# Kernel optimization log

Hardware: AMD Instinct MI355X
Metric: run time of the kernel (lower is better)

The kernel has to match this reference:

```python
import math
import jax, jax.numpy as jnp
import numpy as np

B, T, E = 1, 4096, 768
H, D = 12, 64
RA_WINDOW = 512
INIT_GATES = (2.2, 0.6, 0.1)


def setup_inputs() -> dict:
    key = jax.random.key(0)
    ks = jax.random.split(key, 6)
    x = jax.random.normal(ks[0], (B, T, E), dtype=jnp.float32)
    # Linear weights stored as [in, out] (math-equivalent to torch's x @ W.T)
    s = 1.0 / math.sqrt(E)
    Wq = jax.random.normal(ks[1], (E, H * D), dtype=jnp.float32) * s
    Wk = jax.random.normal(ks[2], (E, H * D), dtype=jnp.float32) * s
    Wv = jax.random.normal(ks[3], (E, H * D), dtype=jnp.float32) * s
    Wo = jax.random.normal(ks[4], (H * D, E), dtype=jnp.float32) * s
    gates = jnp.tile(jnp.asarray(INIT_GATES, dtype=jnp.float32)[None, :], (H, 1))  # [H,3]
    u = jax.random.normal(ks[5], (H, D), dtype=jnp.float32) * 0.02
    return {"x": x, "Wq": Wq, "Wk": Wk, "Wv": Wv, "Wo": Wo, "gates": gates, "u": u}


def reference(x, Wq, Wk, Wv, Wo, gates, u):
    # projections -> [B,H,T,D]
    def proj(W):
        return (x @ W).reshape(B, T, H, D).transpose(0, 2, 1, 3)
    Q, K, V = proj(Wq), proj(Wk), proj(Wv)

    S = jnp.einsum('bhtd,bhsd->bhts', Q, K) / math.sqrt(D)  # [B,H,T,T]

    w = jax.nn.softmax(gates, axis=-1)  # [H,3]
    w_std = w[:, 0][None, :, None, None]
    w_rec = w[:, 1][None, :, None, None]
    w_disc = w[:, 2][None, :, None, None]

    logits = w_std * S + w_rec * jnp.swapaxes(S, -2, -1)

    # discoverability column bias from K via per-head u
    d_raw = jnp.einsum('bhtd,hd->bht', K, u)
    d = d_raw - jnp.mean(d_raw, axis=-1, keepdims=True)
    logits = logits + w_disc * d[:, :, None, :]

    # causal banded mask
    idx = jnp.arange(T)
    mask = (idx[None, :] <= idx[:, None]) & (jnp.abs(idx[None, :] - idx[:, None]) <= RA_WINDOW)
    logits = jnp.where(mask[None, None, :, :], logits, -jnp.inf)

    attn = jax.nn.softmax(logits, axis=-1)
    ctx = jnp.einsum('bhts,bhsd->bhtd', attn, V)
    out = ctx.transpose(0, 2, 1, 3).reshape(B, T, H * D) @ Wo
    return (out, attn)
```

## Files before the change

kernel.cpp:

```cpp
#include <hip/hip_runtime.h>
#include <cstddef>

#define T_LEN 4096
#define EMB 768
#define NH 12
#define HD 64
#define WIN 512

#define GBM 128
#define GBN 128
#define GBK 16

__global__ __launch_bounds__(256) void gemm3_f32(const float* __restrict__ A,
                                                 const float* __restrict__ B0,
                                                 const float* __restrict__ B1,
                                                 const float* __restrict__ B2,
                                                 float* __restrict__ C0,
                                                 float* __restrict__ C1,
                                                 float* __restrict__ C2,
                                                 int M, int N, int K) {
    __shared__ float As[GBK][GBM + 4];
    __shared__ float Bs[GBK][GBN + 4];
    const int tid = threadIdx.x;
    const int bm = blockIdx.y * GBM;
    const int bn = blockIdx.x * GBN;
    const float* __restrict__ B = (blockIdx.z == 0) ? B0 : (blockIdx.z == 1) ? B1 : B2;
    float* __restrict__ C = (blockIdx.z == 0) ? C0 : (blockIdx.z == 1) ? C1 : C2;

    const int ty = (tid >> 4) << 2;
    const int tx = (tid & 15) << 2;

    const int ar = tid >> 1;
    const int ac = (tid & 1) << 3;
    const int br = tid >> 4;
    const int bc = (tid & 15) << 3;

    float acc[8][8] = {};

    for (int k0 = 0; k0 < K; k0 += GBK) {
        const float4 a0 = *(const float4*)&A[(size_t)(bm + ar) * K + k0 + ac];
        const float4 a1 = *(const float4*)&A[(size_t)(bm + ar) * K + k0 + ac + 4];
        As[ac + 0][ar] = a0.x; As[ac + 1][ar] = a0.y; As[ac + 2][ar] = a0.z; As[ac + 3][ar] = a0.w;
        As[ac + 4][ar] = a1.x; As[ac + 5][ar] = a1.y; As[ac + 6][ar] = a1.z; As[ac + 7][ar] = a1.w;
        *(float4*)&Bs[br][bc]     = *(const float4*)&B[(size_t)(k0 + br) * N + bn + bc];
        *(float4*)&Bs[br][bc + 4] = *(const float4*)&B[(size_t)(k0 + br) * N + bn + bc + 4];
        __syncthreads();
#pragma unroll
        for (int k = 0; k < GBK; ++k) {
            const float4 a0v = *(const float4*)&As[k][ty];
            const float4 a1v = *(const float4*)&As[k][ty + 64];
            const float4 b0v = *(const float4*)&Bs[k][tx];
            const float4 b1v = *(const float4*)&Bs[k][tx + 64];
            const float av[8] = {a0v.x, a0v.y, a0v.z, a0v.w, a1v.x, a1v.y, a1v.z, a1v.w};
            const float bv[8] = {b0v.x, b0v.y, b0v.z, b0v.w, b1v.x, b1v.y, b1v.z, b1v.w};
#pragma unroll
            for (int i = 0; i < 8; ++i)
#pragma unroll
                for (int j = 0; j < 8; ++j)
                    acc[i][j] += av[i] * bv[j];
        }
        __syncthreads();
    }
#pragma unroll
    for (int i = 0; i < 8; ++i) {
        const int r = bm + ty + ((i < 4) ? i : (60 + i));
        *(float4*)&C[(size_t)r * N + bn + tx]      = make_float4(acc[i][0], acc[i][1], acc[i][2], acc[i][3]);
        *(float4*)&C[(size_t)r * N + bn + tx + 64] = make_float4(acc[i][4], acc[i][5], acc[i][6], acc[i][7]);
    }
}

__global__ __launch_bounds__(256) void dbias_kernel(const float* __restrict__ K,
                                                    const float* __restrict__ u,
                                                    float* __restrict__ d_bias) {
    const int h = blockIdx.x;
    const int tid = threadIdx.x;
    __shared__ __align__(16) float us[HD];
    __shared__ float dr[T_LEN];
    __shared__ float red[256];
    if (tid < HD) us[tid] = u[h * HD + tid];
    __syncthreads();
    const float4* u4 = (const float4*)us;
    float lsum = 0.f;
    for (int t = tid; t < T_LEN; t += 256) {
        const float4* Kp = (const float4*)&K[(size_t)t * EMB + h * HD];
        float acc = 0.f;
#pragma unroll
        for (int i = 0; i < HD / 4; ++i) {
            float4 k4 = Kp[i];
            float4 uu = u4[i];
            acc += k4.x * uu.x + k4.y * uu.y + k4.z * uu.z + k4.w * uu.w;
        }
        dr[t] = acc;
        lsum += acc;
    }
    red[tid] = lsum;
    __syncthreads();
    for (int off = 128; off > 0; off >>= 1) {
        if (tid < off) red[tid] += red[tid + off];
        __syncthreads();
    }
    const float mean = red[0] * (1.0f / (float)T_LEN);
    __syncthreads();
    for (int t = tid; t < T_LEN; t += 256) {
        d_bias[h * T_LEN + t] = dr[t] - mean;
    }
}

__global__ __launch_bounds__(256) void attn_band_kernel(const float* __restrict__ Q,
                                                        const float* __restrict__ K,
                                                        const float* __restrict__ V,
                                                        const float* __restrict__ d_bias,
                                                        const float* __restrict__ gates,
                                                        float* __restrict__ attn,
                                                        float* __restrict__ ctx,
                                                        float* __restrict__ row_max,
                                                        float* __restrict__ row_invden) {
    const int t0  = blockIdx.x << 6;
    const int h   = blockIdx.y;
    const int tid = threadIdx.x;
    const int tm  = (tid >> 4) << 2;
    const int tn4 = (tid & 15) << 2;
    const int lm  = tid >> 2;
    const int lk  = (tid & 3) << 2;

    __shared__ __align__(16) float QT[64][68];
    __shared__ __align__(16) float KT[64][68];
    __shared__ __align__(16) float Cc[64][68];
    __shared__ __align__(16) float Qs[64][68];

    const float g0 = gates[h * 3 + 0];
    const float g1 = gates[h * 3 + 1];
    const float g2 = gates[h * 3 + 2];
    const float gm = fmaxf(g0, fmaxf(g1, g2));
    const float e0 = __expf(g0 - gm), e1 = __expf(g1 - gm), e2 = __expf(g2 - gm);
    const float gi = 1.0f / (e0 + e1 + e2);
    const float w_std = e0 * gi * 0.125f;
    const float w_rec = e1 * gi * 0.125f;
    const float w_disc = e2 * gi;

    {
        const float* Qp = Q + (size_t)(t0 + lm) * EMB + h * HD + lk;
        const float* Kp = K + (size_t)(t0 + lm) * EMB + h * HD + lk;
#pragma unroll
        for (int it = 0; it < 4; ++it) {
            float4 a = *(const float4*)(Qp + 16 * it);
            QT[lk + 16 * it + 0][lm] = a.x;
            QT[lk + 16 * it + 1][lm] = a.y;
            QT[lk + 16 * it + 2][lm] = a.z;
            QT[lk + 16 * it + 3][lm] = a.w;
            float4 b = *(const float4*)(Kp + 16 * it);
            KT[lk + 16 * it + 0][lm] = b.x;
            KT[lk + 16 * it + 1][lm] = b.y;
            KT[lk + 16 * it + 2][lm] = b.z;
            KT[lk + 16 * it + 3][lm] = b.w;
        }
    }

    const int s_base = (t0 - WIN > 0) ? (t0 - WIN) : 0;
    const int nch = ((t0 + 64) - s_base) >> 6;

    float rm[4], rden[4], acc[4][4];
#pragma unroll
    for (int i = 0; i < 4; ++i) {
        rm[i] = -1e30f;
        rden[i] = 0.f;
#pragma unroll
        for (int j = 0; j < 4; ++j) acc[i][j] = 0.f;
    }

    for (int c = 0; c < nch; ++c) {
        const int s0 = s_base + (c << 6);
        __syncthreads();
        {
            const float* Kp = K + (size_t)(s0 + lm) * EMB + h * HD + lk;
            const float* Qp = Q + (size_t)(s0 + lm) * EMB + h * HD + lk;
#pragma unroll
            for (int it = 0; it < 4; ++it) {
                float4 b = *(const float4*)(Kp + 16 * it);
                Cc[lk + 16 * it + 0][lm] = b.x;
                Cc[lk + 16 * it + 1][lm] = b.y;
                Cc[lk + 16 * it + 2][lm] = b.z;
                Cc[lk + 16 * it + 3][lm] = b.w;
                float4 q = *(const float4*)(Qp + 16 * it);
                Qs[lk + 16 * it + 0][lm] = q.x;
                Qs[lk + 16 * it + 1][lm] = q.y;
                Qs[lk + 16 * it + 2][lm] = q.z;
                Qs[lk + 16 * it + 3][lm] = q.w;
            }
        }
        __syncthreads();

        float m1[4][4] = {};
        float m2[4][4] = {};
#pragma unroll 8
        for (int k = 0; k < 64; ++k) {
            const float4 aq = *(const float4*)&QT[k][tm];
            const float4 bk = *(const float4*)&Cc[k][tn4];
            const float4 ak = *(const float4*)&KT[k][tm];
            const float4 bq = *(const float4*)&Qs[k][tn4];
            m1[0][0] += aq.x * bk.x; m1[0][1] += aq.x * bk.y; m1[0][2] += aq.x * bk.z; m1[0][3] += aq.x * bk.w;
            m1[1][0] += aq.y * bk.x; m1[1][1] += aq.y * bk.y; m1[1][2] += aq.y * bk.z; m1[1][3] += aq.y * bk.w;
            m1[2][0] += aq.z * bk.x; m1[2][1] += aq.z * bk.y; m1[2][2] += aq.z * bk.z; m1[2][3] += aq.z * bk.w;
            m1[3][0] += aq.w * bk.x; m1[3][1] += aq.w * bk.y; m1[3][2] += aq.w * bk.z; m1[3][3] += aq.w * bk.w;
            m2[0][0] += ak.x * bq.x; m2[0][1] += ak.x * bq.y; m2[0][2] += ak.x * bq.z; m2[0][3] += ak.x * bq.w;
            m2[1][0] += ak.y * bq.x; m2[1][1] += ak.y * bq.y; m2[1][2] += ak.y * bq.z; m2[1][3] += ak.y * bq.w;
            m2[2][0] += ak.z * bq.x; m2[2][1] += ak.z * bq.y; m2[2][2] += ak.z * bq.z; m2[2][3] += ak.z * bq.w;
            m2[3][0] += ak.w * bq.x; m2[3][1] += ak.w * bq.y; m2[3][2] += ak.w * bq.z; m2[3][3] += ak.w * bq.w;
        }

        const float4 db = *(const float4*)&d_bias[h * T_LEN + s0 + tn4];
        float l[4][4];
#pragma unroll
        for (int i = 0; i < 4; ++i) {
            const int t = t0 + tm + i;
            const float dbv[4] = {db.x, db.y, db.z, db.w};
#pragma unroll
            for (int j = 0; j < 4; ++j) {
                const int s = s0 + tn4 + j;
                float lv = w_std * m1[i][j] + w_rec * m2[i][j] + w_disc * dbv[j];
                const bool valid = (s <= t) && (s >= t - WIN);
                l[i][j] = valid ? lv : -1e30f;
            }
            *(float4*)&attn[((size_t)(h * T_LEN + t)) * T_LEN + s0 + tn4] =
                make_float4(l[i][0], l[i][1], l[i][2], l[i][3]);
        }
        float cmx[4];
#pragma unroll
        for (int i = 0; i < 4; ++i)
            cmx[i] = fmaxf(fmaxf(l[i][0], l[i][1]), fmaxf(l[i][2], l[i][3]));
#pragma unroll
        for (int off = 1; off < 16; off <<= 1) {
#pragma unroll
            for (int i = 0; i < 4; ++i) cmx[i] = fmaxf(cmx[i], __shfl_xor(cmx[i], off));
        }
        float cs[4];
#pragma unroll
        for (int i = 0; i < 4; ++i) {
            const float nm = fmaxf(rm[i], cmx[i]);
            const float f = __expf(rm[i] - nm);
            float s = 0.f;
#pragma unroll
            for (int j = 0; j < 4; ++j) {
                const float p = __expf(l[i][j] - nm);
                l[i][j] = p;
                s += p;
            }
            cs[i] = s;
            rm[i] = nm;
            rden[i] *= f;
#pragma unroll
            for (int j = 0; j < 4; ++j) acc[i][j] *= f;
        }
#pragma unroll
        for (int off = 1; off < 16; off <<= 1) {
#pragma unroll
            for (int i = 0; i < 4; ++i) cs[i] += __shfl_xor(cs[i], off);
        }
#pragma unroll
        for (int i = 0; i < 4; ++i) rden[i] += cs[i];

        __syncthreads();
#pragma unroll
        for (int i = 0; i < 4; ++i)
#pragma unroll
            for (int j = 0; j < 4; ++j)
                Cc[tn4 + j][tm + i] = l[i][j];
        {
            const float* Vp = V + (size_t)(s0 + lm) * EMB + h * HD + lk;
#pragma unroll
            for (int it = 0; it < 4; ++it)
                *(float4*)&Qs[lm][lk + 16 * it] = *(const float4*)(Vp + 16 * it);
        }
        __syncthreads();

#pragma unroll 16
        for (int k = 0; k < 64; ++k) {
            const float4 av = *(const float4*)&Cc[k][tm];
            const float4 bv = *(const float4*)&Qs[k][tn4];
            acc[0][0] += av.x * bv.x; acc[0][1] += av.x * bv.y; acc[0][2] += av.x * bv.z; acc[0][3] += av.x * bv.w;
            acc[1][0] += av.y * bv.x; acc[1][1] += av.y * bv.y; acc[1][2] += av.y * bv.z; acc[1][3] += av.y * bv.w;
            acc[2][0] += av.z * bv.x; acc[2][1] += av.z * bv.y; acc[2][2] += av.z * bv.z; acc[2][3] += av.z * bv.w;
            acc[3][0] += av.w * bv.x; acc[3][1] += av.w * bv.y; acc[3][2] += av.w * bv.z; acc[3][3] += av.w * bv.w;
        }
    }

#pragma unroll
    for (int i = 0; i < 4; ++i) {
        const float idv = 1.0f / rden[i];
        *(float4*)&ctx[(size_t)(t0 + tm + i) * EMB + h * HD + tn4] =
            make_float4(acc[i][0] * idv, acc[i][1] * idv, acc[i][2] * idv, acc[i][3] * idv);
        if ((tid & 15) == 0) {
            row_max[h * T_LEN + t0 + tm + i] = rm[i];
            row_invden[h * T_LEN + t0 + tm + i] = idv;
        }
    }
}

__global__ __launch_bounds__(256) void attn_norm_kernel(float* __restrict__ attn,
                                                        const float* __restrict__ row_max,
                                                        const float* __restrict__ row_invden) {
    const int t = blockIdx.x;
    const int h = blockIdx.y;
    const float m   = row_max[h * T_LEN + t];
    const float idv = row_invden[h * T_LEN + t];
    float* arow = attn + ((size_t)(h * T_LEN + t)) * T_LEN;
    const int bl = (t - WIN > 0) ? (t - WIN) : 0;
    for (int i4 = threadIdx.x << 2; i4 < T_LEN; i4 += 1024) {
        float4 v = make_float4(0.f, 0.f, 0.f, 0.f);
        if (i4 + 3 >= bl && i4 <= t) {
            const float4 r = *(const float4*)&arow[i4];
            v.x = (i4 + 0 >= bl && i4 + 0 <= t) ? __expf(r.x - m) * idv : 0.f;
            v.y = (i4 + 1 >= bl && i4 + 1 <= t) ? __expf(r.y - m) * idv : 0.f;
            v.z = (i4 + 2 >= bl && i4 + 2 <= t) ? __expf(r.z - m) * idv : 0.f;
            v.w = (i4 + 3 >= bl && i4 + 3 <= t) ? __expf(r.w - m) * idv : 0.f;
        }
        *(float4*)&arow[i4] = v;
    }
}

extern "C" void kernel_launch(void* const* d_in, const int* in_sizes, int n_in,
                              void* d_out, int out_size, void* d_ws, size_t ws_size,
                              hipStream_t stream) {
    const float* x     = (const float*)d_in[0];
    const float* Wq    = (const float*)d_in[1];
    const float* Wk    = (const float*)d_in[2];
    const float* Wv    = (const float*)d_in[3];
    const float* Wo    = (const float*)d_in[4];
    const float* gates = (const float*)d_in[5];
    const float* u     = (const float*)d_in[6];

    float* out  = (float*)d_out;
    float* attn = out + (size_t)T_LEN * EMB;

    float* ws = (float*)d_ws;
    float* Qb = ws;
    float* Kb = Qb + (size_t)T_LEN * EMB;
    float* Vb = Kb + (size_t)T_LEN * EMB;
    float* Cb = Vb + (size_t)T_LEN * EMB;
    float* Db = Cb + (size_t)T_LEN * EMB;
    float* Mb = Db + (size_t)NH * T_LEN;
    float* Ib = Mb + (size_t)NH * T_LEN;

    gemm3_f32<<<dim3(EMB / GBN, T_LEN / GBM, 3), 256, 0, stream>>>(
        x, Wq, Wk, Wv, Qb, Kb, Vb, T_LEN, EMB, EMB);
    dbias_kernel<<<NH, 256, 0, stream>>>(Kb, u, Db);

    attn_band_kernel<<<dim3(T_LEN / 64, NH), 256, 0, stream>>>(Qb, Kb, Vb, Db, gates,
                                                               attn, Cb, Mb, Ib);
    attn_norm_kernel<<<dim3(T_LEN, NH), 256, 0, stream>>>(attn, Mb, Ib);

    gemm3_f32<<<dim3(EMB / GBN, T_LEN / GBM, 1), 256, 0, stream>>>(
        Cb, Wo, Wo, Wo, out, out, out, T_LEN, EMB, EMB);
}
```

Before: 1.459 ms.

## Fuse attention normalization into band kernel and prefetch tiles into registers

Removes the separate attn_norm pass. The band kernel now keeps each chunk's running max in shared memory, stores logits already shifted by the per-chunk max, and at the end rescales its own band tiles by a per-chunk correction factor. It also zero-fills the out-of-band columns itself. K/Q/V chunk loads in the band kernel and A/B tile loads in the GEMM are software-prefetched into registers one iteration ahead. This avoids a full extra read and write pass over the 12x4096x4096 attn matrix, at the cost of more registers and shared memory.

```diff
diff --git a/kernel.cpp b/kernel.cpp
--- a/kernel.cpp
+++ b/kernel.cpp
@@ -37,14 +37,23 @@
 
     float acc[8][8] = {};
 
+    float4 pa0 = *(const float4*)&A[(size_t)(bm + ar) * K + ac];
+    float4 pa1 = *(const float4*)&A[(size_t)(bm + ar) * K + ac + 4];
+    float4 pb0 = *(const float4*)&B[(size_t)br * N + bn + bc];
+    float4 pb1 = *(const float4*)&B[(size_t)br * N + bn + bc + 4];
+
     for (int k0 = 0; k0 < K; k0 += GBK) {
-        const float4 a0 = *(const float4*)&A[(size_t)(bm + ar) * K + k0 + ac];
-        const float4 a1 = *(const float4*)&A[(size_t)(bm + ar) * K + k0 + ac + 4];
-        As[ac + 0][ar] = a0.x; As[ac + 1][ar] = a0.y; As[ac + 2][ar] = a0.z; As[ac + 3][ar] = a0.w;
-        As[ac + 4][ar] = a1.x; As[ac + 5][ar] = a1.y; As[ac + 6][ar] = a1.z; As[ac + 7][ar] = a1.w;
-        *(float4*)&Bs[br][bc]     = *(const float4*)&B[(size_t)(k0 + br) * N + bn + bc];
-        *(float4*)&Bs[br][bc + 4] = *(const float4*)&B[(size_t)(k0 + br) * N + bn + bc + 4];
-        __syncthreads();
+        As[ac + 0][ar] = pa0.x; As[ac + 1][ar] = pa0.y; As[ac + 2][ar] = pa0.z; As[ac + 3][ar] = pa0.w;
+        As[ac + 4][ar] = pa1.x; As[ac + 5][ar] = pa1.y; As[ac + 6][ar] = pa1.z; As[ac + 7][ar] = pa1.w;
+        *(float4*)&Bs[br][bc]     = pb0;
+        *(float4*)&Bs[br][bc + 4] = pb1;
+        __syncthreads();
+        if (k0 + GBK < K) {
+            pa0 = *(const float4*)&A[(size_t)(bm + ar) * K + k0 + GBK + ac];
+            pa1 = *(const float4*)&A[(size_t)(bm + ar) * K + k0 + GBK + ac + 4];
+            pb0 = *(const float4*)&B[(size_t)(k0 + GBK + br) * N + bn + bc];
+            pb1 = *(const float4*)&B[(size_t)(k0 + GBK + br) * N + bn + bc + 4];
+        }
 #pragma unroll
         for (int k = 0; k < GBK; ++k) {
             const float4 a0v = *(const float4*)&As[k][ty];
@@ -112,9 +121,7 @@
                                                         const float* __restrict__ d_bias,
                                                         const float* __restrict__ gates,
                                                         float* __restrict__ attn,
-                                                        float* __restrict__ ctx,
-                                                        float* __restrict__ row_max,
-                                                        float* __restrict__ row_invden) {
+                                                        float* __restrict__ ctx) {
     const int t0  = blockIdx.x << 6;
     const int h   = blockIdx.y;
     const int tid = threadIdx.x;
@@ -127,6 +134,9 @@
     __shared__ __align__(16) float KT[64][68];
     __shared__ __align__(16) float Cc[64][68];
     __shared__ __align__(16) float Qs[64][68];
+    __shared__ float cm[9][64];
+    __shared__ float rmf[64];
+    __shared__ float idvf[64];
 
     const float g0 = gates[h * 3 + 0];
     const float g1 = gates[h * 3 + 1];
@@ -168,27 +178,46 @@
         for (int j = 0; j < 4; ++j) acc[i][j] = 0.f;
     }
 
+    float4 kr[4], qr[4], vcur[4], vnxt[4];
+    {
+        const float* Kp = K + (size_t)(s_base + lm) * EMB + h * HD + lk;
+        const float* Qp = Q + (size_t)(s_base + lm) * EMB + h * HD + lk;
+        const float* Vp = V + (size_t)(s_base + lm) * EMB + h * HD + lk;
+#pragma unroll
+        for (int it = 0; it < 4; ++it) {
+            kr[it]   = *(const float4*)(Kp + 16 * it);
+            qr[it]   = *(const float4*)(Qp + 16 * it);
+            vcur[it] = *(const float4*)(Vp + 16 * it);
+        }
+    }
+
     for (int c = 0; c < nch; ++c) {
         const int s0 = s_base + (c << 6);
         __syncthreads();
-        {
-            const float* Kp = K + (size_t)(s0 + lm) * EMB + h * HD + lk;
-            const float* Qp = Q + (size_t)(s0 + lm) * EMB + h * HD + lk;
+#pragma unroll
+        for (int it = 0; it < 4; ++it) {
+            Cc[lk + 16 * it + 0][lm] = kr[it].x;
+            Cc[lk + 16 * it + 1][lm] = kr[it].y;
+            Cc[lk + 16 * it + 2][lm] = kr[it].z;
+            Cc[lk + 16 * it + 3][lm] = kr[it].w;
+            Qs[lk + 16 * it + 0][lm] = qr[it].x;
+            Qs[lk + 16 * it + 1][lm] = qr[it].y;
+            Qs[lk + 16 * it + 2][lm] = qr[it].z;
+            Qs[lk + 16 * it + 3][lm] = qr[it].w;
+        }
+        __syncthreads();
+        if (c + 1 < nch) {
+            const int s1 = s0 + 64;
+            const float* Kp = K + (size_t)(s1 + lm) * EMB + h * HD + lk;
+            const float* Qp = Q + (size_t)(s1 + lm) * EMB + h * HD + lk;
+            const float* Vp = V + (size_t)(s1 + lm) * EMB + h * HD + lk;
 #pragma unroll
             for (int it = 0; it < 4; ++it) {
-                float4 b = *(const float4*)(Kp + 16 * it);
-                Cc[lk + 16 * it + 0][lm] = b.x;
-                Cc[lk + 16 * it + 1][lm] = b.y;
-                Cc[lk + 16 * it + 2][lm] = b.z;
-                Cc[lk + 16 * it + 3][lm] = b.w;
-                float4 q = *(const float4*)(Qp + 16 * it);
-                Qs[lk + 16 * it + 0][lm] = q.x;
-                Qs[lk + 16 * it + 1][lm] = q.y;
-                Qs[lk + 16 * it + 2][lm] = q.z;
-                Qs[lk + 16 * it + 3][lm] = q.w;
+                kr[it]   = *(const float4*)(Kp + 16 * it);
+                qr[it]   = *(const float4*)(Qp + 16 * it);
+                vnxt[it] = *(const float4*)(Vp + 16 * it);
             }
         }
-        __syncthreads();
 
         float m1[4][4] = {};
         float m2[4][4] = {};
@@ -221,8 +250,6 @@
                 const bool valid = (s <= t) && (s >= t - WIN);
                 l[i][j] = valid ? lv : -1e30f;
             }
-            *(float4*)&attn[((size_t)(h * T_LEN + t)) * T_LEN + s0 + tn4] =
-                make_float4(l[i][0], l[i][1], l[i][2], l[i][3]);
         }
         float cmx[4];
 #pragma unroll
@@ -250,6 +277,9 @@
             rden[i] *= f;
 #pragma unroll
             for (int j = 0; j < 4; ++j) acc[i][j] *= f;
+            *(float4*)&attn[((size_t)(h * T_LEN + t0 + tm + i)) * T_LEN + s0 + tn4] =
+                make_float4(l[i][0], l[i][1], l[i][2], l[i][3]);
+            if ((tid & 15) == 0) cm[c][tm + i] = nm;
         }
 #pragma unroll
         for (int off = 1; off < 16; off <<= 1) {
@@ -265,12 +295,9 @@
 #pragma unroll
             for (int j = 0; j < 4; ++j)
                 Cc[tn4 + j][tm + i] = l[i][j];
-        {
-            const float* Vp = V + (size_t)(s0 + lm) * EMB + h * HD + lk;
-#pragma unroll
-            for (int it = 0; it < 4; ++it)
-                *(float4*)&Qs[lm][lk + 16 * it] = *(const float4*)(Vp + 16 * it);
-        }
+#pragma unroll
+        for (int it = 0; it < 4; ++it)
+            *(float4*)&Qs[lm][lk + 16 * it] = vcur[it];
         __syncthreads();
 
 #pragma unroll 16
@@ -282,39 +309,49 @@
             acc[2][0] += av.z * bv.x; acc[2][1] += av.z * bv.y; acc[2][2] += av.z * bv.z; acc[2][3] += av.z * bv.w;
             acc[3][0] += av.w * bv.x; acc[3][1] += av.w * bv.y; acc[3][2] += av.w * bv.z; acc[3][3] += av.w * bv.w;
         }
-    }
-
+#pragma unroll
+        for (int it = 0; it < 4; ++it) vcur[it] = vnxt[it];
+    }
+
+    float idv[4];
 #pragma unroll
     for (int i = 0; i < 4; ++i) {
-        const float idv = 1.0f / rden[i];
+        idv[i] = 1.0f / rden[i];
         *(float4*)&ctx[(size_t)(t0 + tm + i) * EMB + h * HD + tn4] =
-            make_float4(acc[i][0] * idv, acc[i][1] * idv, acc[i][2] * idv, acc[i][3] * idv);
-        if ((tid & 15) == 0) {
-            row_max[h * T_LEN + t0 + tm + i] = rm[i];
-            row_invden[h * T_LEN + t0 + tm + i] = idv;
-        }
-    }
-}
-
-__global__ __launch_bounds__(256) void attn_norm_kernel(float* __restrict__ attn,
-                                                        const float* __restrict__ row_max,
-                                                        const float* __restrict__ row_invden) {
-    const int t = blockIdx.x;
-    const int h = blockIdx.y;
-    const float m   = row_max[h * T_LEN + t];
-    const float idv = row_invden[h * T_LEN + t];
-    float* arow = attn + ((size_t)(h * T_LEN + t)) * T_LEN;
-    const int bl = (t - WIN > 0) ? (t - WIN) : 0;
-    for (int i4 = threadIdx.x << 2; i4 < T_LEN; i4 += 1024) {
-        float4 v = make_float4(0.f, 0.f, 0.f, 0.f);
-        if (i4 + 3 >= bl && i4 <= t) {
-            const float4 r = *(const float4*)&arow[i4];
-            v.x = (i4 + 0 >= bl && i4 + 0 <= t) ? __expf(r.x - m) * idv : 0.f;
-            v.y = (i4 + 1 >= bl && i4 + 1 <= t) ? __expf(r.y - m) * idv : 0.f;
-            v.z = (i4 + 2 >= bl && i4 + 2 <= t) ? __expf(r.z - m) * idv : 0.f;
-            v.w = (i4 + 3 >= bl && i4 + 3 <= t) ? __expf(r.w - m) * idv : 0.f;
-        }
-        *(float4*)&arow[i4] = v;
+            make_float4(acc[i][0] * idv[i], acc[i][1] * idv[i], acc[i][2] * idv[i], acc[i][3] * idv[i]);
+    }
+    if ((tid & 15) == 0) {
+#pragma unroll
+        for (int i = 0; i < 4; ++i) {
+            rmf[tm + i] = rm[i];
+            idvf[tm + i] = idv[i];
+        }
+    }
+    __syncthreads();
+    for (int idx = tid; idx < (nch << 6); idx += 256) {
+        const int c = idx >> 6, r = idx & 63;
+        cm[c][r] = __expf(cm[c][r] - rmf[r]) * idvf[r];
+    }
+    __syncthreads();
+    for (int c = 0; c < nch; ++c) {
+        const int s0 = s_base + (c << 6);
+#pragma unroll
+        for (int i = 0; i < 4; ++i) {
+            float* p = &attn[((size_t)(h * T_LEN + t0 + tm + i)) * T_LEN + s0 + tn4];
+            const float f = cm[c][tm + i];
+            const float4 v = *(const float4*)p;
+            *(float4*)p = make_float4(v.x * f, v.y * f, v.z * f, v.w * f);
+        }
+    }
+    const int s_end = s_base + (nch << 6);
+    const int wv = tid >> 6, ln = tid & 63;
+    const float4 z4 = make_float4(0.f, 0.f, 0.f, 0.f);
+    for (int r = wv; r < 64; r += 4) {
+        float* arow = attn + ((size_t)(h * T_LEN + t0 + r)) * T_LEN;
+        for (int col = ln << 2; col < s_base; col += 256)
+            *(float4*)&arow[col] = z4;
+        for (int col = s_end + (ln << 2); col < T_LEN; col += 256)
+            *(float4*)&arow[col] = z4;
     }
 }
 
@@ -338,16 +375,13 @@
     float* Vb = Kb + (size_t)T_LEN * EMB;
     float* Cb = Vb + (size_t)T_LEN * EMB;
     float* Db = Cb + (size_t)T_LEN * EMB;
-    float* Mb = Db + (size_t)NH * T_LEN;
-    float* Ib = Mb + (size_t)NH * T_LEN;
 
     gemm3_f32<<<dim3(EMB / GBN, T_LEN / GBM, 3), 256, 0, stream>>>(
         x, Wq, Wk, Wv, Qb, Kb, Vb, T_LEN, EMB, EMB);
     dbias_kernel<<<NH, 256, 0, stream>>>(Kb, u, Db);
 
     attn_band_kernel<<<dim3(T_LEN / 64, NH), 256, 0, stream>>>(Qb, Kb, Vb, Db, gates,
-                                                               attn, Cb, Mb, Ib);
-    attn_norm_kernel<<<dim3(T_LEN, NH), 256, 0, stream>>>(attn, Mb, Ib);
+                                                               attn, Cb);
 
     gemm3_f32<<<dim3(EMB / GBN, T_LEN / GBM, 1), 256, 0, stream>>>(
         Cb, Wo, Wo, Wo, out, out, out, T_LEN, EMB, EMB);
```

New measurement: 1.499 ms. +2.7%, slower.
